# Performance work log

Hardware: AMD Instinct MI355X
Metric: run time of the kernel (lower is better)

## Reference

```python
import jax, jax.numpy as jnp
import numpy as np

N = 100000
E = 1600000


def gcn_conv(x, W, b, src, dst, n_nodes):
    """PyG GCNConv: linear -> add self loops -> sym-normalized scatter-add."""
    h = x @ W  # [N, out]
    # degree with self-loops: deg[i] = 1 + in_degree(i)
    deg = jax.ops.segment_sum(jnp.ones((src.shape[0],), h.dtype), dst,
                              num_segments=n_nodes) + 1.0
    dinv = jax.lax.rsqrt(deg)  # deg >= 1 always
    norm = dinv[src] * dinv[dst]  # [E]
    # neighbor messages + self-loop contribution (norm = deg^-1)
    agg = jax.ops.segment_sum(h[src] * norm[:, None], dst,
                              num_segments=n_nodes)
    return agg + h * (dinv * dinv)[:, None] + b


def setup_inputs() -> dict:
    key = jax.random.key(0)
    k1, k2, k3, k4 = jax.random.split(key, 4)
    x = jax.random.normal(k1, (N, 128), dtype=jnp.float32)
    edge_index = jax.random.randint(k2, (2, E), 0, N, dtype=jnp.int64)
    W1 = jax.random.normal(k3, (128, 64), dtype=jnp.float32) * (1.0 / np.sqrt(128))
    b1 = jnp.zeros((64,), jnp.float32)
    W2 = jax.random.normal(k4, (64, 40), dtype=jnp.float32) * (1.0 / np.sqrt(64))
    b2 = jnp.zeros((40,), jnp.float32)
    return {"x": x, "edge_index": edge_index, "W1": W1, "b1": b1,
            "W2": W2, "b2": b2}


def reference(x, edge_index, W1, b1, W2, b2):
    src, dst = edge_index[0], edge_index[1]
    h = gcn_conv(x, W1, b1, src, dst, N)
    h = jax.nn.relu(h)
    # dropout is identity in eval mode; mask_features is a no-op
    h = gcn_conv(h, W2, b2, src, dst, N)
    return jax.nn.log_softmax(h, axis=1)
```

## Files before the change

### kernel.cpp

```cpp
#include <hip/hip_runtime.h>
#include <math.h>

#define N_NODES 100000
#define N_EDGES 1600000
#define F_IN    128
#define F_HID   64
#define F_OUT   40

#define BIN_SHIFT 8
#define NBINS     392
#define BIN_CAP   5120
#define FILL_BLOCKS 512
#define GEMM1_BLOCKS ((N_NODES + 63) / 64)

typedef unsigned int  uint;
typedef unsigned short ushort;
typedef __attribute__((ext_vector_type(8))) short bf16x8;
typedef __attribute__((ext_vector_type(4))) float f32x4;

__device__ __forceinline__ unsigned short f2bf(float f) {
    uint u = __float_as_uint(f);
    u = (u + 0x7FFF + ((u >> 16) & 1)) >> 16;
    return (unsigned short)u;
}
__device__ __forceinline__ uint pack2bf(float a, float b) {
    return (uint)f2bf(a) | ((uint)f2bf(b) << 16);
}
__device__ __forceinline__ float bf_lo(uint u) { return __uint_as_float(u << 16); }
__device__ __forceinline__ float bf_hi(uint u) { return __uint_as_float(u & 0xFFFF0000u); }

__global__ void prep_kernel(const float* __restrict__ W, uint* __restrict__ Wt,
                            int* __restrict__ bcursor) {
    int tid = threadIdx.x;
    if (tid < NBINS) bcursor[tid] = tid * BIN_CAP;
    for (int i = tid; i < 4096; i += 512) {
        int c  = i >> 6;
        int kp = i & 63;
        Wt[i] = pack2bf(W[(2 * kp) * F_HID + c], W[(2 * kp + 1) * F_HID + c]);
    }
}

#define XPITCH 68
__global__ __launch_bounds__(256) void fillgemm_kernel(
        const int* __restrict__ src, const int* __restrict__ dst,
        int* __restrict__ bcursor, int* __restrict__ bins, int E,
        const float* __restrict__ x, const uint* __restrict__ Wt,
        ushort* __restrict__ h, int n) {
    __shared__ __align__(16) uint smem[2 * 64 * XPITCH];
    int tid = threadIdx.x;

    if (blockIdx.x < FILL_BLOCKS) {
        int* lcount = (int*)smem;
        int* gbase  = ((int*)smem) + NBINS;
        for (int i = tid; i < NBINS; i += 256) lcount[i] = 0;
        __syncthreads();
        int chunk = (E + FILL_BLOCKS - 1) / FILL_BLOCKS;
        int beg = blockIdx.x * chunk, end = min(E, beg + chunk);
        for (int e = beg + tid; e < end; e += 256)
            atomicAdd(&lcount[dst[e] >> BIN_SHIFT], 1);
        __syncthreads();
        for (int i = tid; i < NBINS; i += 256) {
            gbase[i] = lcount[i] ? atomicAdd(&bcursor[i], lcount[i]) : 0;
            lcount[i] = 0;
        }
        __syncthreads();
        for (int e = beg + tid; e < end; e += 256) {
            int d = dst[e];
            int b = d >> BIN_SHIFT;
            int p = atomicAdd(&lcount[b], 1);
            bins[gbase[b] + p] = src[e] | ((d & 255) << 17);
        }
        return;
    }

    uint* Xu = smem;
    uint* Wu = smem + 64 * XPITCH;
    int node0 = (blockIdx.x - FILL_BLOCKS) * 64;

    {
        int c = tid >> 2, qq = tid & 3;
        const uint4* gsrc = (const uint4*)&Wt[c * 64 + qq * 16];
        uint4* ldst = (uint4*)&Wu[c * XPITCH + qq * 16];
        #pragma unroll
        for (int j = 0; j < 4; ++j) ldst[j] = gsrc[j];
    }
    {
        int row = tid >> 2, qq = tid & 3;
        int node = node0 + row;
        uint4* ldst = (uint4*)&Xu[row * XPITCH + qq * 16];
        if (node < n) {
            const float4* gsrc = (const float4*)&x[(size_t)node * F_IN + qq * 32];
            #pragma unroll
            for (int j = 0; j < 4; ++j) {
                float4 a = gsrc[2 * j], b = gsrc[2 * j + 1];
                uint4 o;
                o.x = pack2bf(a.x, a.y); o.y = pack2bf(a.z, a.w);
                o.z = pack2bf(b.x, b.y); o.w = pack2bf(b.z, b.w);
                ldst[j] = o;
            }
        } else {
            uint4 z = make_uint4(0, 0, 0, 0);
            #pragma unroll
            for (int j = 0; j < 4; ++j) ldst[j] = z;
        }
    }
    __syncthreads();

    int wv   = tid >> 6;
    int lane = tid & 63;
    int lrow = lane & 15;
    int quad = lane >> 4;

    bf16x8 bfrag[4][4];
    #pragma unroll
    for (int t = 0; t < 4; ++t)
        #pragma unroll
        for (int s = 0; s < 4; ++s)
            bfrag[t][s] = *(const bf16x8*)&Wu[(t * 16 + lrow) * XPITCH + s * 16 + quad * 4];

    f32x4 acc[4];
    #pragma unroll
    for (int t = 0; t < 4; ++t) acc[t] = (f32x4){0.f, 0.f, 0.f, 0.f};

    #pragma unroll
    for (int s = 0; s < 4; ++s) {
        bf16x8 afrag = *(const bf16x8*)&Xu[(wv * 16 + lrow) * XPITCH + s * 16 + quad * 4];
        #pragma unroll
        for (int t = 0; t < 4; ++t)
            acc[t] = __builtin_amdgcn_mfma_f32_16x16x32_bf16(afrag, bfrag[t][s], acc[t], 0, 0, 0);
    }

    #pragma unroll
    for (int t = 0; t < 4; ++t) {
        #pragma unroll
        for (int i = 0; i < 4; ++i) {
            int node = node0 + wv * 16 + quad * 4 + i;
            if (node < n) h[(size_t)node * F_HID + t * 16 + lrow] = f2bf(acc[t][i]);
        }
    }
}

__global__ void binsort_kernel(const int* __restrict__ bcursor, const int* __restrict__ bins,
                               int* __restrict__ csr, int* __restrict__ rowstart,
                               int* __restrict__ rowcnt, float* __restrict__ dinv) {
    __shared__ int hist[256];
    __shared__ int scan[256];
    __shared__ int cur[256];
    __shared__ int sorted[BIN_CAP];
    int b = blockIdx.x, t = threadIdx.x;
    int base = b * BIN_CAP;
    int cnt = bcursor[b] - base;
    if (t < 256) hist[t] = 0;
    __syncthreads();
    for (int i = t; i < cnt; i += 512)
        atomicAdd(&hist[(unsigned)bins[base + i] >> 17], 1);
    __syncthreads();
    int v = 0;
    if (t < 256) { v = hist[t]; scan[t] = v; }
    __syncthreads();
    for (int off = 1; off < 256; off <<= 1) {
        int u = (t < 256 && t >= off) ? scan[t - off] : 0;
        __syncthreads();
        if (t < 256) scan[t] += u;
        __syncthreads();
    }
    if (t < 256) {
        int excl = scan[t] - v;
        cur[t] = excl;
        int node = (b << BIN_SHIFT) + t;
        if (node < N_NODES) {
            rowstart[node] = base + excl;
            rowcnt[node]   = v;
            dinv[node] = rsqrtf((float)v + 1.0f);
        }
    }
    __syncthreads();
    for (int i = t; i < cnt; i += 512) {
        int p   = bins[base + i];
        int pos = atomicAdd(&cur[(unsigned)p >> 17], 1);
        sorted[pos] = p & 0x1FFFF;
    }
    __syncthreads();
    for (int i = t; i < cnt; i += 512)
        csr[base + i] = sorted[i];
}

__global__ void agg1_kernel(const int* __restrict__ rowstart, const int* __restrict__ rowcnt,
                            const int* __restrict__ csr, const float* __restrict__ dinv,
                            const ushort* __restrict__ h, const float* __restrict__ b,
                            ushort* __restrict__ out, int n) {
    int node = blockIdx.x * 4 + (threadIdx.x >> 6);
    int lane = threadIdx.x & 63;
    if (node >= n) return;
    int slot = lane >> 3;
    int c    = lane & 7;
    int beg = rowstart[node], end = beg + rowcnt[node];
    float acc[8] = {0.f,0.f,0.f,0.f,0.f,0.f,0.f,0.f};
    for (int base = beg; base < end; base += 64) {
        int idx = base + lane;
        int   sid = 0; float wgt = 0.f;
        if (idx < end) { sid = csr[idx]; wgt = dinv[sid]; }
        int cnt    = min(64, end - base);
        int groups = (cnt + 7) >> 3;
        int g = 0;
        for (; g + 2 <= groups; g += 2) {
            int   sA = __shfl(sid, g * 8 + slot);
            float wA = __shfl(wgt, g * 8 + slot);
            int   sB = __shfl(sid, g * 8 + 8 + slot);
            float wB = __shfl(wgt, g * 8 + 8 + slot);
            uint4 hA = *(const uint4*)&h[(size_t)sA * F_HID + (c << 3)];
            uint4 hB = *(const uint4*)&h[(size_t)sB * F_HID + (c << 3)];
            acc[0] += bf_lo(hA.x) * wA; acc[1] += bf_hi(hA.x) * wA;
            acc[2] += bf_lo(hA.y) * wA; acc[3] += bf_hi(hA.y) * wA;
            acc[4] += bf_lo(hA.z) * wA; acc[5] += bf_hi(hA.z) * wA;
            acc[6] += bf_lo(hA.w) * wA; acc[7] += bf_hi(hA.w) * wA;
            acc[0] += bf_lo(hB.x) * wB; acc[1] += bf_hi(hB.x) * wB;
            acc[2] += bf_lo(hB.y) * wB; acc[3] += bf_hi(hB.y) * wB;
            acc[4] += bf_lo(hB.z) * wB; acc[5] += bf_hi(hB.z) * wB;
            acc[6] += bf_lo(hB.w) * wB; acc[7] += bf_hi(hB.w) * wB;
        }
        if (g < groups) {
            int   sA = __shfl(sid, g * 8 + slot);
            float wA = __shfl(wgt, g * 8 + slot);
            uint4 hA = *(const uint4*)&h[(size_t)sA * F_HID + (c << 3)];
            acc[0] += bf_lo(hA.x) * wA; acc[1] += bf_hi(hA.x) * wA;
            acc[2] += bf_lo(hA.y) * wA; acc[3] += bf_hi(hA.y) * wA;
            acc[4] += bf_lo(hA.z) * wA; acc[5] += bf_hi(hA.z) * wA;
            acc[6] += bf_lo(hA.w) * wA; acc[7] += bf_hi(hA.w) * wA;
        }
    }
    #pragma unroll
    for (int m = 8; m < 64; m <<= 1) {
        #pragma unroll
        for (int k = 0; k < 8; ++k) acc[k] += __shfl_xor(acc[k], m);
    }
    if (slot == 0) {
        float di = dinv[node];
        uint4 hs = *(const uint4*)&h[(size_t)node * F_HID + (c << 3)];
        float self[8] = { bf_lo(hs.x), bf_hi(hs.x), bf_lo(hs.y), bf_hi(hs.y),
                          bf_lo(hs.z), bf_hi(hs.z), bf_lo(hs.w), bf_hi(hs.w) };
        float4 b0 = *(const float4*)&b[c << 3];
        float4 b1v = *(const float4*)&b[(c << 3) + 4];
        float bb[8] = { b0.x, b0.y, b0.z, b0.w, b1v.x, b1v.y, b1v.z, b1v.w };
        ushort o[8];
        #pragma unroll
        for (int k = 0; k < 8; ++k) {
            float v = fmaxf(acc[k] * di + self[k] * di * di + bb[k], 0.f);
            o[k] = f2bf(v);
        }
        uint4 pk;
        pk.x = (uint)o[0] | ((uint)o[1] << 16);
        pk.y = (uint)o[2] | ((uint)o[3] << 16);
        pk.z = (uint)o[4] | ((uint)o[5] << 16);
        pk.w = (uint)o[6] | ((uint)o[7] << 16);
        *(uint4*)&out[(size_t)node * F_HID + (c << 3)] = pk;
    }
}

__global__ void gemm2_kernel(const ushort* __restrict__ a, const float* __restrict__ W,
                             ushort* __restrict__ h, int n) {
    __shared__ float Wl[F_HID * F_OUT];
    int tid = threadIdx.x;
    for (int i = tid; i < F_HID * F_OUT; i += 256) Wl[i] = W[i];
    __syncthreads();
    long long idx = (long long)blockIdx.x * 256 + tid;
    if (idx >= (long long)n * F_OUT) return;
    int node = (int)(idx / F_OUT);
    int col  = (int)(idx - (long long)node * F_OUT);
    const uint* arow = (const uint*)(a + (size_t)node * F_HID);
    float acc = 0.0f;
    #pragma unroll 8
    for (int k = 0; k < F_HID / 2; ++k) {
        uint u = arow[k];
        acc += bf_lo(u) * Wl[(2 * k) * F_OUT + col] + bf_hi(u) * Wl[(2 * k + 1) * F_OUT + col];
    }
    h[idx] = f2bf(acc);
}

__global__ void agg2_kernel(const int* __restrict__ rowstart, const int* __restrict__ rowcnt,
                            const int* __restrict__ csr, const float* __restrict__ dinv,
                            const ushort* __restrict__ h, const float* __restrict__ b,
                            float* __restrict__ out, int n) {
    int node = blockIdx.x * 4 + (threadIdx.x >> 6);
    int lane = threadIdx.x & 63;
    if (node >= n) return;
    int slot = lane / 10;
    int c    = lane - slot * 10;
    int beg = rowstart[node], end = beg + rowcnt[node];
    float acc[4] = {0.f, 0.f, 0.f, 0.f};
    for (int base = beg; base < end; base += 60) {
        int idx = base + lane;
        int   sid = 0; float wgt = 0.f;
        if (lane < 60 && idx < end) { sid = csr[idx]; wgt = dinv[sid]; }
        int cnt    = min(60, end - base);
        int groups = (cnt + 5) / 6;
        int g = 0;
        for (; g + 2 <= groups; g += 2) {
            int   slA = (slot < 6) ? (g * 6 + slot) : 60;
            int   slB = (slot < 6) ? (g * 6 + 6 + slot) : 60;
            int   sA = __shfl(sid, slA);
            float wA = __shfl(wgt, slA);
            int   sB = __shfl(sid, slB);
            float wB = __shfl(wgt, slB);
            uint2 hA = *(const uint2*)&h[(size_t)sA * F_OUT + (c << 2)];
            uint2 hB = *(const uint2*)&h[(size_t)sB * F_OUT + (c << 2)];
            acc[0] += bf_lo(hA.x) * wA; acc[1] += bf_hi(hA.x) * wA;
            acc[2] += bf_lo(hA.y) * wA; acc[3] += bf_hi(hA.y) * wA;
            acc[0] += bf_lo(hB.x) * wB; acc[1] += bf_hi(hB.x) * wB;
            acc[2] += bf_lo(hB.y) * wB; acc[3] += bf_hi(hB.y) * wB;
        }
        if (g < groups) {
            int   slA = (slot < 6) ? (g * 6 + slot) : 60;
            int   sA = __shfl(sid, slA);
            float wA = __shfl(wgt, slA);
            uint2 hA = *(const uint2*)&h[(size_t)sA * F_OUT + (c << 2)];
            acc[0] += bf_lo(hA.x) * wA; acc[1] += bf_hi(hA.x) * wA;
            acc[2] += bf_lo(hA.y) * wA; acc[3] += bf_hi(hA.y) * wA;
        }
    }
    float r[4];
    #pragma unroll
    for (int k = 0; k < 4; ++k) {
        float t3 = __shfl(acc[k], lane + 30);
        float s0 = acc[k] + t3;
        float t1 = __shfl(s0, lane + 10);
        float t2 = __shfl(s0, lane + 20);
        r[k] = s0 + t1 + t2;
    }
    float val[4] = {0.f, 0.f, 0.f, 0.f};
    float m = -INFINITY;
    if (lane < 10) {
        float di = dinv[node];
        uint2 hs = *(const uint2*)&h[(size_t)node * F_OUT + (c << 2)];
        float self[4] = { bf_lo(hs.x), bf_hi(hs.x), bf_lo(hs.y), bf_hi(hs.y) };
        float4 bb = *(const float4*)&b[c << 2];
        float bbv[4] = { bb.x, bb.y, bb.z, bb.w };
        #pragma unroll
        for (int k = 0; k < 4; ++k) {
            val[k] = r[k] * di + self[k] * di * di + bbv[k];
            m = fmaxf(m, val[k]);
        }
    }
    #pragma unroll
    for (int off = 1; off < 16; off <<= 1) m = fmaxf(m, __shfl_xor(m, off));
    float p = 0.f;
    if (lane < 10)
        p = __expf(val[0] - m) + __expf(val[1] - m) + __expf(val[2] - m) + __expf(val[3] - m);
    #pragma unroll
    for (int off = 1; off < 16; off <<= 1) p += __shfl_xor(p, off);
    float lse = m + __logf(p);
    if (lane < 10) {
        float4 o;
        o.x = val[0] - lse; o.y = val[1] - lse; o.z = val[2] - lse; o.w = val[3] - lse;
        *(float4*)&out[(size_t)node * F_OUT + (c << 2)] = o;
    }
}

extern "C" void kernel_launch(void* const* d_in, const int* in_sizes, int n_in,
                              void* d_out, int out_size, void* d_ws, size_t ws_size,
                              hipStream_t stream) {
    const float* x  = (const float*)d_in[0];
    const int*   ei = (const int*)d_in[1];
    const float* W1 = (const float*)d_in[2];
    const float* b1 = (const float*)d_in[3];
    const float* W2 = (const float*)d_in[4];
    const float* b2 = (const float*)d_in[5];
    const int* src = ei;
    const int* dst = ei + N_EDGES;

    char* p = (char*)d_ws;
    int*    bcursor  = (int*)p;     p += (size_t)(NBINS + 8) * 4;
    int*    bins     = (int*)p;     p += (size_t)NBINS * BIN_CAP * 4;
    int*    csr_src  = (int*)p;     p += (size_t)NBINS * BIN_CAP * 4;
    int*    rowstart = (int*)p;     p += (size_t)(N_NODES + 4) * 4;
    int*    rowcnt   = (int*)p;     p += (size_t)(N_NODES + 4) * 4;
    float*  dinv     = (float*)p;   p += (size_t)N_NODES * 4;
    uint*   Wtb      = (uint*)p;    p += (size_t)4096 * 4;
    ushort* h1b      = (ushort*)p;  p += (size_t)N_NODES * F_HID * 2;
    ushort* out1b    = (ushort*)p;  p += (size_t)N_NODES * F_HID * 2;
    ushort* h2b      = (ushort*)p;  p += (size_t)N_NODES * F_OUT * 2;
    float*  out      = (float*)d_out;

    prep_kernel    <<<1, 512, 0, stream>>>(W1, Wtb, bcursor);
    fillgemm_kernel<<<FILL_BLOCKS + GEMM1_BLOCKS, 256, 0, stream>>>(
        src, dst, bcursor, bins, N_EDGES, x, Wtb, h1b, N_NODES);
    binsort_kernel <<<NBINS, 512, 0, stream>>>(bcursor, bins, csr_src, rowstart, rowcnt, dinv);
    agg1_kernel    <<<(N_NODES + 3) / 4, 256, 0, stream>>>(rowstart, rowcnt, csr_src, dinv,
                                                           h1b, b1, out1b, N_NODES);
    gemm2_kernel   <<<((N_NODES * F_OUT) + 255) / 256, 256, 0, stream>>>(out1b, W2, h2b, N_NODES);
    agg2_kernel    <<<(N_NODES + 3) / 4, 256, 0, stream>>>(rowstart, rowcnt, csr_src, dinv,
                                                           h2b, b2, out, N_NODES);
}
```

Measured before the change: 280.0 us.

## Map four nodes per wavefront in aggregation, pad layer-2 features, switch to fp16

Both aggregation kernels now give each node 16 lanes instead of a full 64-lane wavefront, so one wavefront handles four nodes. This is meant to cut idle lanes and the cross-lane reductions for low-degree nodes, which average about 16 edges here. The layer-2 hidden tensor is padded from 40 to 64 columns so agg2 can reuse the 16-byte gather path, at the cost of extra memory traffic and extra writes in gemm2. Intermediate storage and the MFMA input type change from bf16 to fp16, which trades exponent range for mantissa precision and could risk overflow.

```diff
diff --git a/kernel.cpp b/kernel.cpp
--- a/kernel.cpp
+++ b/kernel.cpp
@@ -1,4 +1,5 @@
 #include <hip/hip_runtime.h>
+#include <hip/hip_fp16.h>
 #include <math.h>
 
 #define N_NODES 100000
@@ -12,22 +13,28 @@
 #define BIN_CAP   5120
 #define FILL_BLOCKS 512
 #define GEMM1_BLOCKS ((N_NODES + 63) / 64)
+#define AGG_BLOCKS  ((N_NODES + 15) / 16)
 
 typedef unsigned int  uint;
 typedef unsigned short ushort;
-typedef __attribute__((ext_vector_type(8))) short bf16x8;
+typedef __attribute__((ext_vector_type(8))) _Float16 half8;
 typedef __attribute__((ext_vector_type(4))) float f32x4;
 
-__device__ __forceinline__ unsigned short f2bf(float f) {
-    uint u = __float_as_uint(f);
-    u = (u + 0x7FFF + ((u >> 16) & 1)) >> 16;
-    return (unsigned short)u;
-}
-__device__ __forceinline__ uint pack2bf(float a, float b) {
-    return (uint)f2bf(a) | ((uint)f2bf(b) << 16);
-}
-__device__ __forceinline__ float bf_lo(uint u) { return __uint_as_float(u << 16); }
-__device__ __forceinline__ float bf_hi(uint u) { return __uint_as_float(u & 0xFFFF0000u); }
+__device__ __forceinline__ uint pack2h(float a, float b) {
+    __half2 h = __floats2half2_rn(a, b);
+    return *(const uint*)&h;
+}
+__device__ __forceinline__ ushort f2h(float f) {
+    return __half_as_ushort(__float2half_rn(f));
+}
+__device__ __forceinline__ void fma8(float* acc, uint4 hv, float w) {
+    const __half2* hp = (const __half2*)&hv;
+    #pragma unroll
+    for (int j = 0; j < 4; ++j) {
+        acc[2 * j]     = fmaf(__low2float(hp[j]),  w, acc[2 * j]);
+        acc[2 * j + 1] = fmaf(__high2float(hp[j]), w, acc[2 * j + 1]);
+    }
+}
 
 __global__ void prep_kernel(const float* __restrict__ W, uint* __restrict__ Wt,
                             int* __restrict__ bcursor) {
@@ -36,7 +43,7 @@
     for (int i = tid; i < 4096; i += 512) {
         int c  = i >> 6;
         int kp = i & 63;
-        Wt[i] = pack2bf(W[(2 * kp) * F_HID + c], W[(2 * kp + 1) * F_HID + c]);
+        Wt[i] = pack2h(W[(2 * kp) * F_HID + c], W[(2 * kp + 1) * F_HID + c]);
     }
 }
 
@@ -94,8 +101,8 @@
             for (int j = 0; j < 4; ++j) {
                 float4 a = gsrc[2 * j], b = gsrc[2 * j + 1];
                 uint4 o;
-                o.x = pack2bf(a.x, a.y); o.y = pack2bf(a.z, a.w);
-                o.z = pack2bf(b.x, b.y); o.w = pack2bf(b.z, b.w);
+                o.x = pack2h(a.x, a.y); o.y = pack2h(a.z, a.w);
+                o.z = pack2h(b.x, b.y); o.w = pack2h(b.z, b.w);
                 ldst[j] = o;
             }
         } else {
@@ -111,12 +118,12 @@
     int lrow = lane & 15;
     int quad = lane >> 4;
 
-    bf16x8 bfrag[4][4];
+    half8 bfrag[4][4];
     #pragma unroll
     for (int t = 0; t < 4; ++t)
         #pragma unroll
         for (int s = 0; s < 4; ++s)
-            bfrag[t][s] = *(const bf16x8*)&Wu[(t * 16 + lrow) * XPITCH + s * 16 + quad * 4];
+            bfrag[t][s] = *(const half8*)&Wu[(t * 16 + lrow) * XPITCH + s * 16 + quad * 4];
 
     f32x4 acc[4];
     #pragma unroll
@@ -124,10 +131,10 @@
 
     #pragma unroll
     for (int s = 0; s < 4; ++s) {
-        bf16x8 afrag = *(const bf16x8*)&Xu[(wv * 16 + lrow) * XPITCH + s * 16 + quad * 4];
+        half8 afrag = *(const half8*)&Xu[(wv * 16 + lrow) * XPITCH + s * 16 + quad * 4];
         #pragma unroll
         for (int t = 0; t < 4; ++t)
-            acc[t] = __builtin_amdgcn_mfma_f32_16x16x32_bf16(afrag, bfrag[t][s], acc[t], 0, 0, 0);
+            acc[t] = __builtin_amdgcn_mfma_f32_16x16x32_f16(afrag, bfrag[t][s], acc[t], 0, 0, 0);
     }
 
     #pragma unroll
@@ -135,7 +142,7 @@
         #pragma unroll
         for (int i = 0; i < 4; ++i) {
             int node = node0 + wv * 16 + quad * 4 + i;
-            if (node < n) h[(size_t)node * F_HID + t * 16 + lrow] = f2bf(acc[t][i]);
+            if (node < n) h[(size_t)node * F_HID + t * 16 + lrow] = f2h(acc[t][i]);
         }
     }
 }
@@ -189,70 +196,59 @@
                             const int* __restrict__ csr, const float* __restrict__ dinv,
                             const ushort* __restrict__ h, const float* __restrict__ b,
                             ushort* __restrict__ out, int n) {
-    int node = blockIdx.x * 4 + (threadIdx.x >> 6);
     int lane = threadIdx.x & 63;
+    int sub  = lane >> 4;
+    int l16  = lane & 15;
+    int slot = l16 >> 3;
+    int c    = l16 & 7;
+    int node = blockIdx.x * 16 + (threadIdx.x >> 6) * 4 + sub;
     if (node >= n) return;
-    int slot = lane >> 3;
-    int c    = lane & 7;
     int beg = rowstart[node], end = beg + rowcnt[node];
+    int lbase = (lane & 48) + slot;
     float acc[8] = {0.f,0.f,0.f,0.f,0.f,0.f,0.f,0.f};
-    for (int base = beg; base < end; base += 64) {
-        int idx = base + lane;
+    for (int base = beg; base < end; base += 16) {
+        int idx = base + l16;
         int   sid = 0; float wgt = 0.f;
         if (idx < end) { sid = csr[idx]; wgt = dinv[sid]; }
-        int cnt    = min(64, end - base);
-        int groups = (cnt + 7) >> 3;
+        int m = min(16, end - base);
+        int groups = (m + 1) >> 1;
         int g = 0;
         for (; g + 2 <= groups; g += 2) {
-            int   sA = __shfl(sid, g * 8 + slot);
-            float wA = __shfl(wgt, g * 8 + slot);
-            int   sB = __shfl(sid, g * 8 + 8 + slot);
-            float wB = __shfl(wgt, g * 8 + 8 + slot);
+            int   sA = __shfl(sid, lbase + 2 * g);
+            float wA = __shfl(wgt, lbase + 2 * g);
+            int   sB = __shfl(sid, lbase + 2 * g + 2);
+            float wB = __shfl(wgt, lbase + 2 * g + 2);
             uint4 hA = *(const uint4*)&h[(size_t)sA * F_HID + (c << 3)];
             uint4 hB = *(const uint4*)&h[(size_t)sB * F_HID + (c << 3)];
-            acc[0] += bf_lo(hA.x) * wA; acc[1] += bf_hi(hA.x) * wA;
-            acc[2] += bf_lo(hA.y) * wA; acc[3] += bf_hi(hA.y) * wA;
-            acc[4] += bf_lo(hA.z) * wA; acc[5] += bf_hi(hA.z) * wA;
-            acc[6] += bf_lo(hA.w) * wA; acc[7] += bf_hi(hA.w) * wA;
-            acc[0] += bf_lo(hB.x) * wB; acc[1] += bf_hi(hB.x) * wB;
-            acc[2] += bf_lo(hB.y) * wB; acc[3] += bf_hi(hB.y) * wB;
-            acc[4] += bf_lo(hB.z) * wB; acc[5] += bf_hi(hB.z) * wB;
-            acc[6] += bf_lo(hB.w) * wB; acc[7] += bf_hi(hB.w) * wB;
+            fma8(acc, hA, wA);
+            fma8(acc, hB, wB);
         }
         if (g < groups) {
-            int   sA = __shfl(sid, g * 8 + slot);
-            float wA = __shfl(wgt, g * 8 + slot);
+            int   sA = __shfl(sid, lbase + 2 * g);
+            float wA = __shfl(wgt, lbase + 2 * g);
             uint4 hA = *(const uint4*)&h[(size_t)sA * F_HID + (c << 3)];
-            acc[0] += bf_lo(hA.x) * wA; acc[1] += bf_hi(hA.x) * wA;
-            acc[2] += bf_lo(hA.y) * wA; acc[3] += bf_hi(hA.y) * wA;
-            acc[4] += bf_lo(hA.z) * wA; acc[5] += bf_hi(hA.z) * wA;
-            acc[6] += bf_lo(hA.w) * wA; acc[7] += bf_hi(hA.w) * wA;
-        }
-    }
-    #pragma unroll
-    for (int m = 8; m < 64; m <<= 1) {
-        #pragma unroll
-        for (int k = 0; k < 8; ++k) acc[k] += __shfl_xor(acc[k], m);
-    }
+            fma8(acc, hA, wA);
+        }
+    }
+    #pragma unroll
+    for (int k = 0; k < 8; ++k) acc[k] += __shfl_xor(acc[k], 8);
     if (slot == 0) {
-        float di = dinv[node];
+        float di  = dinv[node];
+        float di2 = di * di;
         uint4 hs = *(const uint4*)&h[(size_t)node * F_HID + (c << 3)];
-        float self[8] = { bf_lo(hs.x), bf_hi(hs.x), bf_lo(hs.y), bf_hi(hs.y),
-                          bf_lo(hs.z), bf_hi(hs.z), bf_lo(hs.w), bf_hi(hs.w) };
-        float4 b0 = *(const float4*)&b[c << 3];
+        const __half2* hp = (const __half2*)&hs;
+        float4 b0  = *(const float4*)&b[c << 3];
         float4 b1v = *(const float4*)&b[(c << 3) + 4];
         float bb[8] = { b0.x, b0.y, b0.z, b0.w, b1v.x, b1v.y, b1v.z, b1v.w };
-        ushort o[8];
-        #pragma unroll
-        for (int k = 0; k < 8; ++k) {
-            float v = fmaxf(acc[k] * di + self[k] * di * di + bb[k], 0.f);
-            o[k] = f2bf(v);
+        float v[8];
+        #pragma unroll
+        for (int k = 0; k < 4; ++k) {
+            v[2*k]   = fmaxf(fmaf(acc[2*k],   di, __low2float(hp[k])  * di2) + bb[2*k],   0.f);
+            v[2*k+1] = fmaxf(fmaf(acc[2*k+1], di, __high2float(hp[k]) * di2) + bb[2*k+1], 0.f);
         }
         uint4 pk;
-        pk.x = (uint)o[0] | ((uint)o[1] << 16);
-        pk.y = (uint)o[2] | ((uint)o[3] << 16);
-        pk.z = (uint)o[4] | ((uint)o[5] << 16);
-        pk.w = (uint)o[6] | ((uint)o[7] << 16);
+        pk.x = pack2h(v[0], v[1]); pk.y = pack2h(v[2], v[3]);
+        pk.z = pack2h(v[4], v[5]); pk.w = pack2h(v[6], v[7]);
         *(uint4*)&out[(size_t)node * F_HID + (c << 3)] = pk;
     }
 }
@@ -263,96 +259,100 @@
     int tid = threadIdx.x;
     for (int i = tid; i < F_HID * F_OUT; i += 256) Wl[i] = W[i];
     __syncthreads();
-    long long idx = (long long)blockIdx.x * 256 + tid;
-    if (idx >= (long long)n * F_OUT) return;
-    int node = (int)(idx / F_OUT);
-    int col  = (int)(idx - (long long)node * F_OUT);
-    const uint* arow = (const uint*)(a + (size_t)node * F_HID);
+    int idx = blockIdx.x * 256 + tid;
+    if (idx >= n * 64) return;
+    int node = idx >> 6;
+    int col  = idx & 63;
     float acc = 0.0f;
-    #pragma unroll 8
-    for (int k = 0; k < F_HID / 2; ++k) {
-        uint u = arow[k];
-        acc += bf_lo(u) * Wl[(2 * k) * F_OUT + col] + bf_hi(u) * Wl[(2 * k + 1) * F_OUT + col];
-    }
-    h[idx] = f2bf(acc);
+    if (col < F_OUT) {
+        const uint* arow = (const uint*)(a + (size_t)node * F_HID);
+        #pragma unroll 8
+        for (int k = 0; k < F_HID / 2; ++k) {
+            uint u = arow[k];
+            __half2 hv = *(const __half2*)&u;
+            acc = fmaf(__low2float(hv),  Wl[(2 * k) * F_OUT + col], acc);
+            acc = fmaf(__high2float(hv), Wl[(2 * k + 1) * F_OUT + col], acc);
+        }
+    }
+    h[(size_t)node * 64 + col] = f2h(col < F_OUT ? acc : 0.0f);
 }
 
 __global__ void agg2_kernel(const int* __restrict__ rowstart, const int* __restrict__ rowcnt,
                             const int* __restrict__ csr, const float* __restrict__ dinv,
                             const ushort* __restrict__ h, const float* __restrict__ b,
                             float* __restrict__ out, int n) {
-    int node = blockIdx.x * 4 + (threadIdx.x >> 6);
     int lane = threadIdx.x & 63;
+    int sub  = lane >> 4;
+    int l16  = lane & 15;
+    int slot = l16 >> 3;
+    int c    = l16 & 7;
+    int node = blockIdx.x * 16 + (threadIdx.x >> 6) * 4 + sub;
     if (node >= n) return;
-    int slot = lane / 10;
-    int c    = lane - slot * 10;
     int beg = rowstart[node], end = beg + rowcnt[node];
-    float acc[4] = {0.f, 0.f, 0.f, 0.f};
-    for (int base = beg; base < end; base += 60) {
-        int idx = base + lane;
+    int lbase = (lane & 48) + slot;
+    float acc[8] = {0.f,0.f,0.f,0.f,0.f,0.f,0.f,0.f};
+    for (int base = beg; base < end; base += 16) {
+        int idx = base + l16;
         int   sid = 0; float wgt = 0.f;
-        if (lane < 60 && idx < end) { sid = csr[idx]; wgt = dinv[sid]; }
-        int cnt    = min(60, end - base);
-        int groups = (cnt + 5) / 6;
+        if (idx < end) { sid = csr[idx]; wgt = dinv[sid]; }
+        int m = min(16, end - base);
+        int groups = (m + 1) >> 1;
         int g = 0;
         for (; g + 2 <= groups; g += 2) {
-            int   slA = (slot < 6) ? (g * 6 + slot) : 60;
-            int   slB = (slot < 6) ? (g * 6 + 6 + slot) : 60;
-            int   sA = __shfl(sid, slA);
-            float wA = __shfl(wgt, slA);
-            int   sB = __shfl(sid, slB);
-            float wB = __shfl(wgt, slB);
-            uint2 hA = *(const uint2*)&h[(size_t)sA * F_OUT + (c << 2)];
-            uint2 hB = *(const uint2*)&h[(size_t)sB * F_OUT + (c << 2)];
-            acc[0] += bf_lo(hA.x) * wA; acc[1] += bf_hi(hA.x) * wA;
-            acc[2] += bf_lo(hA.y) * wA; acc[3] += bf_hi(hA.y) * wA;
-            acc[0] += bf_lo(hB.x) * wB; acc[1] += bf_hi(hB.x) * wB;
-            acc[2] += bf_lo(hB.y) * wB; acc[3] += bf_hi(hB.y) * wB;
+            int   sA = __shfl(sid, lbase + 2 * g);
+            float wA = __shfl(wgt, lbase + 2 * g);
+            int   sB = __shfl(sid, lbase + 2 * g + 2);
+            float wB = __shfl(wgt, lbase + 2 * g + 2);
+            uint4 hA = *(const uint4*)&h[(size_t)sA * 64 + (c << 3)];
+            uint4 hB = *(const uint4*)&h[(size_t)sB * 64 + (c << 3)];
+            fma8(acc, hA, wA);
+            fma8(acc, hB, wB);
         }
         if (g < groups) {
-            int   slA = (slot < 6) ? (g * 6 + slot) : 60;
-            int   sA = __shfl(sid, slA);
-            float wA = __shfl(wgt, slA);
-            uint2 hA = *(const uint2*)&h[(size_t)sA * F_OUT + (c << 2)];
-            acc[0] += bf_lo(hA.x) * wA; acc[1] += bf_hi(hA.x) * wA;
-            acc[2] += bf_lo(hA.y) * wA; acc[3] += bf_hi(hA.y) * wA;
-        }
-    }
-    float r[4];
-    #pragma unroll
-    for (int k = 0; k < 4; ++k) {
-        float t3 = __shfl(acc[k], lane + 30);
-        float s0 = acc[k] + t3;
-        float t1 = __shfl(s0, lane + 10);
-        float t2 = __shfl(s0, lane + 20);
-        r[k] = s0 + t1 + t2;
-    }
-    float val[4] = {0.f, 0.f, 0.f, 0.f};
-    float m = -INFINITY;
-    if (lane < 10) {
-        float di = dinv[node];
-        uint2 hs = *(const uint2*)&h[(size_t)node * F_OUT + (c << 2)];
-        float self[4] = { bf_lo(hs.x), bf_hi(hs.x), bf_lo(hs.y), bf_hi(hs.y) };
-        float4 bb = *(const float4*)&b[c << 2];
-        float bbv[4] = { bb.x, bb.y, bb.z, bb.w };
+            int   sA = __shfl(sid, lbase + 2 * g);
+            float wA = __shfl(wgt, lbase + 2 * g);
+            uint4 hA = *(const uint4*)&h[(size_t)sA * 64 + (c << 3)];
+            fma8(acc, hA, wA);
+        }
+    }
+    #pragma unroll
+    for (int k = 0; k < 8; ++k) acc[k] += __shfl_xor(acc[k], 8);
+    bool active = (slot == 0) && (c < 5);
+    float val[8];
+    float mx = -INFINITY;
+    if (active) {
+        float di  = dinv[node];
+        float di2 = di * di;
+        uint4 hs = *(const uint4*)&h[(size_t)node * 64 + (c << 3)];
+        const __half2* hp = (const __half2*)&hs;
+        float4 b0  = *(const float4*)&b[c << 3];
+        float4 b1v = *(const float4*)&b[(c << 3) + 4];
+        float bb[8] = { b0.x, b0.y, b0.z, b0.w, b1v.x, b1v.y, b1v.z, b1v.w };
         #pragma unroll
         for (int k = 0; k < 4; ++k) {
-            val[k] = r[k] * di + self[k] * di * di + bbv[k];
-            m = fmaxf(m, val[k]);
-        }
-    }
-    #pragma unroll
-    for (int off = 1; off < 16; off <<= 1) m = fmaxf(m, __shfl_xor(m, off));
+            val[2*k]   = fmaf(acc[2*k],   di, __low2float(hp[k])  * di2) + bb[2*k];
+            val[2*k+1] = fmaf(acc[2*k+1], di, __high2float(hp[k]) * di2) + bb[2*k+1];
+        }
+        #pragma unroll
+        for (int k = 0; k < 8; ++k) mx = fmaxf(mx, val[k]);
+    }
+    #pragma unroll
+    for (int off = 1; off < 8; off <<= 1) mx = fmaxf(mx, __shfl_xor(mx, off));
     float p = 0.f;
-    if (lane < 10)
-        p = __expf(val[0] - m) + __expf(val[1] - m) + __expf(val[2] - m) + __expf(val[3] - m);
-    #pragma unroll
-    for (int off = 1; off < 16; off <<= 1) p += __shfl_xor(p, off);
-    float lse = m + __logf(p);
-    if (lane < 10) {
-        float4 o;
-        o.x = val[0] - lse; o.y = val[1] - lse; o.z = val[2] - lse; o.w = val[3] - lse;
-        *(float4*)&out[(size_t)node * F_OUT + (c << 2)] = o;
+    if (active) {
+        #pragma unroll
+        for (int k = 0; k < 8; ++k) p += __expf(val[k] - mx);
+    }
+    #pragma unroll
+    for (int off = 1; off < 8; off <<= 1) p += __shfl_xor(p, off);
+    float lse = mx + __logf(p);
+    if (active) {
+        float4 o0, o1;
+        o0.x = val[0] - lse; o0.y = val[1] - lse; o0.z = val[2] - lse; o0.w = val[3] - lse;
+        o1.x = val[4] - lse; o1.y = val[5] - lse; o1.z = val[6] - lse; o1.w = val[7] - lse;
+        float* orow = &out[(size_t)node * F_OUT + (c << 3)];
+        *(float4*)orow       = o0;
+        *(float4*)(orow + 4) = o1;
     }
 }
 
@@ -378,16 +378,16 @@
     uint*   Wtb      = (uint*)p;    p += (size_t)4096 * 4;
     ushort* h1b      = (ushort*)p;  p += (size_t)N_NODES * F_HID * 2;
     ushort* out1b    = (ushort*)p;  p += (size_t)N_NODES * F_HID * 2;
-    ushort* h2b      = (ushort*)p;  p += (size_t)N_NODES * F_OUT * 2;
+    ushort* h2b      = (ushort*)p;  p += ((size_t)N_NODES * 64 + 64) * 2;
     float*  out      = (float*)d_out;
 
     prep_kernel    <<<1, 512, 0, stream>>>(W1, Wtb, bcursor);
     fillgemm_kernel<<<FILL_BLOCKS + GEMM1_BLOCKS, 256, 0, stream>>>(
         src, dst, bcursor, bins, N_EDGES, x, Wtb, h1b, N_NODES);
     binsort_kernel <<<NBINS, 512, 0, stream>>>(bcursor, bins, csr_src, rowstart, rowcnt, dinv);
-    agg1_kernel    <<<(N_NODES + 3) / 4, 256, 0, stream>>>(rowstart, rowcnt, csr_src, dinv,
-                                                           h1b, b1, out1b, N_NODES);
-    gemm2_kernel   <<<((N_NODES * F_OUT) + 255) / 256, 256, 0, stream>>>(out1b, W2, h2b, N_NODES);
-    agg2_kernel    <<<(N_NODES + 3) / 4, 256, 0, stream>>>(rowstart, rowcnt, csr_src, dinv,
-                                                           h2b, b2, out, N_NODES);
-}
+    agg1_kernel    <<<AGG_BLOCKS, 256, 0, stream>>>(rowstart, rowcnt, csr_src, dinv,
+                                                    h1b, b1, out1b, N_NODES);
+    gemm2_kernel   <<<(N_NODES * 64 + 255) / 256, 256, 0, stream>>>(out1b, W2, h2b, N_NODES);
+    agg2_kernel    <<<AGG_BLOCKS, 256, 0, stream>>>(rowstart, rowcnt, csr_src, dinv,
+                                                    h2b, b2, out, N_NODES);
+}
```

New measurement: 299.3 us. 6.9% more time.
